# Performance work log

Measured on AMD Instinct MI355X. Metric: run time of the kernel, lower is better.

Reference implementation:

```python
import jax, jax.numpy as jnp
import numpy as np

N = 262144          # total instances (patches)
E = 512             # encoding_size
H = 256             # attention_hidden_size
NUM_BAGS = 512      # number of bags (slides); max(batch_indices)+1


def setup_inputs() -> dict:
    key = jax.random.key(0)
    k1, k2, k3, k4, k5 = jax.random.split(key, 5)
    bag_encoding = jax.random.normal(k1, (N, E), dtype=jnp.float32)
    idx = jnp.sort(jax.random.randint(k2, (N,), 0, NUM_BAGS))
    # ensure num_bags = max+1 == NUM_BAGS deterministically
    batch_indices = idx.at[0].set(0).at[-1].set(NUM_BAGS - 1)
    # kaiming-uniform-ish fan_in init scales
    Vw = jax.random.uniform(k3, (H, E), jnp.float32, -1.0, 1.0) * np.sqrt(6.0 / E)
    Vb = jnp.zeros((H,), jnp.float32)
    ww = jax.random.uniform(k4, (1, H), jnp.float32, -1.0, 1.0) * np.sqrt(6.0 / H)
    wb = jnp.zeros((1,), jnp.float32)
    dw = jax.random.uniform(k5, (2, E), jnp.float32, -1.0, 1.0) * np.sqrt(6.0 / E)
    db = jnp.zeros((2,), jnp.float32)
    return {"bag_encoding": bag_encoding, "Vw": Vw, "Vb": Vb, "ww": ww,
            "wb": wb, "dw": dw, "db": db, "batch_indices": batch_indices}


def reference(bag_encoding, Vw, Vb, ww, wb, dw, db, batch_indices):
    # attention scores: tanh(V x) -> w -> exp   [N, 1]
    v = jnp.tanh(jnp.einsum('ne,he->nh', bag_encoding, Vw) + Vb)
    alphas = jnp.exp(jnp.einsum('nh,oh->no', v, ww) + wb)  # [N, 1]
    # segment softmax denominator per bag
    sum_alphas = jax.ops.segment_sum(alphas, batch_indices, num_segments=NUM_BAGS)  # [B, 1]
    alphas = alphas / sum_alphas[batch_indices]
    # attention-weighted bag pooling
    bag_sum = jax.ops.segment_sum(alphas * bag_encoding, batch_indices, num_segments=NUM_BAGS)  # [B, E]
    logits = jnp.einsum('be,ce->bc', bag_sum, dw) + db  # [B, 2]
    return jax.nn.softmax(logits, axis=1)
```

## Files before the change

### kernel.cpp

```cpp
#include <hip/hip_runtime.h>
#include <hip/hip_bf16.h>

#define N_INST 262144
#define E_DIM  512
#define H_DIM  256
#define NBAGS  512
#define MI     32
#define XS_STRIDE 520
#define NBLOCKS 256
#define TILES_PER_BLK (N_INST / MI / NBLOCKS)

typedef __bf16 bf16x8 __attribute__((ext_vector_type(8)));
typedef float  f32x4  __attribute__((ext_vector_type(4)));

__device__ __forceinline__ float fast_tanh(float x) {
    float e = __expf(2.0f * x);
    return 1.0f - 2.0f * __builtin_amdgcn_rcpf(e + 1.0f);
}

__global__ void vw_to_bf16(const float* __restrict__ src,
                           __hip_bfloat16* __restrict__ dst) {
    int i = (blockIdx.x * 256 + threadIdx.x) * 4;
    float4 f = *(const float4*)(src + i);
    dst[i + 0] = __float2bfloat16(f.x);
    dst[i + 1] = __float2bfloat16(f.y);
    dst[i + 2] = __float2bfloat16(f.z);
    dst[i + 3] = __float2bfloat16(f.w);
}

__global__ __launch_bounds__(512, 2) void attn_persist(
    const float* __restrict__ X,
    const __hip_bfloat16* __restrict__ Vw,
    const float* __restrict__ Vb,
    const float* __restrict__ ww,
    const float* __restrict__ wb,
    const int* __restrict__ bidx,
    float* __restrict__ bag_acc,
    float* __restrict__ sum_alphas)
{
    __shared__ __hip_bfloat16 xs[2][MI][XS_STRIDE];
    __shared__ float s_part[8][MI];
    __shared__ float a_sh[MI];
    __shared__ int   bag_sh[2][MI];

    const int tid  = threadIdx.x;
    const int wave = tid >> 6;
    const int lane = tid & 63;
    const int l16  = lane & 15;
    const int kgrp = lane >> 4;

    const int tile0 = blockIdx.x * TILES_PER_BLK;

    bf16x8 breg[16][2];
    float ww_r[2], vb_r[2];
    {
        const __bf16* Vwp = (const __bf16*)Vw;
        #pragma unroll
        for (int nt = 0; nt < 2; nt++) {
            const int h = wave * 32 + nt * 16 + l16;
            ww_r[nt] = ww[h];
            vb_r[nt] = Vb[h];
            #pragma unroll
            for (int k = 0; k < 16; k++)
                breg[k][nt] = *(const bf16x8*)(Vwp + (size_t)h * E_DIM + k * 32 + kgrp * 8);
        }
    }

    const int c4 = tid & 127;
    const int r0 = tid >> 7;

    {
        const size_t i0 = (size_t)tile0 * MI;
        #pragma unroll
        for (int rr = 0; rr < 8; rr++) {
            const int r = rr * 4 + r0;
            float4 f = *(const float4*)(X + (i0 + r) * E_DIM + c4 * 4);
            __hip_bfloat16* dst = &xs[0][r][c4 * 4];
            dst[0] = __float2bfloat16(f.x);
            dst[1] = __float2bfloat16(f.y);
            dst[2] = __float2bfloat16(f.z);
            dst[3] = __float2bfloat16(f.w);
        }
        if (tid < MI) bag_sh[0][tid] = bidx[i0 + tid];
    }
    __syncthreads();

    int   cur_bag = -1;
    float col_acc = 0.f;
    float asum    = 0.f;

    int p = 0;
    for (int it = 0; it < TILES_PER_BLK; it++) {
        const size_t inst0 = (size_t)(tile0 + it) * MI;
        const bool has_next = (it + 1 < TILES_PER_BLK);

        float4 ld[8];
        if (has_next) {
            const size_t i1 = inst0 + MI;
            #pragma unroll
            for (int rr = 0; rr < 8; rr++)
                ld[rr] = *(const float4*)(X + (i1 + rr * 4 + r0) * E_DIM + c4 * 4);
        }

        f32x4 acc[2][2];
        #pragma unroll
        for (int mt = 0; mt < 2; mt++)
            #pragma unroll
            for (int nt = 0; nt < 2; nt++)
                acc[mt][nt] = (f32x4){0.f, 0.f, 0.f, 0.f};

        #pragma unroll
        for (int k = 0; k < 16; k++) {
            bf16x8 a_frag[2];
            #pragma unroll
            for (int mt = 0; mt < 2; mt++)
                a_frag[mt] = *(const bf16x8*)&xs[p][mt * 16 + l16][k * 32 + kgrp * 8];
            #pragma unroll
            for (int mt = 0; mt < 2; mt++)
                #pragma unroll
                for (int nt = 0; nt < 2; nt++)
                    acc[mt][nt] = __builtin_amdgcn_mfma_f32_16x16x32_bf16(
                        a_frag[mt], breg[k][nt], acc[mt][nt], 0, 0, 0);
        }

        if (has_next) {
            #pragma unroll
            for (int rr = 0; rr < 8; rr++) {
                const int r = rr * 4 + r0;
                __hip_bfloat16* dst = &xs[p ^ 1][r][c4 * 4];
                dst[0] = __float2bfloat16(ld[rr].x);
                dst[1] = __float2bfloat16(ld[rr].y);
                dst[2] = __float2bfloat16(ld[rr].z);
                dst[3] = __float2bfloat16(ld[rr].w);
            }
            if (tid < MI) bag_sh[p ^ 1][tid] = bidx[inst0 + MI + tid];
        }

        #pragma unroll
        for (int mt = 0; mt < 2; mt++) {
            #pragma unroll
            for (int r = 0; r < 4; r++) {
                float t = 0.f;
                #pragma unroll
                for (int nt = 0; nt < 2; nt++)
                    t += ww_r[nt] * fast_tanh(acc[mt][nt][r] + vb_r[nt]);
                #pragma unroll
                for (int off = 1; off < 16; off <<= 1)
                    t += __shfl_xor(t, off, 64);
                if (l16 == 0)
                    s_part[wave][mt * 16 + kgrp * 4 + r] = t;
            }
        }
        __syncthreads();

        if (tid < MI) {
            float s = wb[0];
            #pragma unroll
            for (int w = 0; w < 8; w++) s += s_part[w][tid];
            a_sh[tid] = __expf(s);
        }
        __syncthreads();

        for (int i = 0; i < MI; i++) {
            const int b = bag_sh[p][i];
            if (b != cur_bag) {
                if (cur_bag >= 0) {
                    atomicAdd(&bag_acc[(size_t)cur_bag * E_DIM + tid], col_acc);
                    if (tid == 0) atomicAdd(&sum_alphas[cur_bag], asum);
                }
                cur_bag = b; col_acc = 0.f; asum = 0.f;
            }
            const float a = a_sh[i];
            col_acc += a * __bfloat162float(xs[p][i][tid]);
            asum    += a;
        }
        __syncthreads();
        p ^= 1;
    }

    if (cur_bag >= 0) {
        atomicAdd(&bag_acc[(size_t)cur_bag * E_DIM + tid], col_acc);
        if (tid == 0) atomicAdd(&sum_alphas[cur_bag], asum);
    }
}

__global__ void finalize(const float* __restrict__ bag_acc,
                         const float* __restrict__ sum_alphas,
                         const float* __restrict__ dw,
                         const float* __restrict__ db,
                         float* __restrict__ out) {
    const int b = blockIdx.x;
    const int lane = threadIdx.x;
    const float sa = sum_alphas[b];
    const float inv = (sa > 0.f) ? (1.f / sa) : 0.f;
    float l0 = 0.f, l1 = 0.f;
    for (int e = lane; e < E_DIM; e += 64) {
        const float bs = bag_acc[(size_t)b * E_DIM + e] * inv;
        l0 += bs * dw[e];
        l1 += bs * dw[E_DIM + e];
    }
    for (int off = 32; off; off >>= 1) {
        l0 += __shfl_xor(l0, off, 64);
        l1 += __shfl_xor(l1, off, 64);
    }
    if (lane == 0) {
        l0 += db[0];
        l1 += db[1];
        const float m  = fmaxf(l0, l1);
        const float e0 = expf(l0 - m), e1 = expf(l1 - m);
        const float is = 1.f / (e0 + e1);
        out[b * 2 + 0] = e0 * is;
        out[b * 2 + 1] = e1 * is;
    }
}

extern "C" void kernel_launch(void* const* d_in, const int* in_sizes, int n_in,
                              void* d_out, int out_size, void* d_ws, size_t ws_size,
                              hipStream_t stream) {
    const float* X   = (const float*)d_in[0];
    const float* Vwf = (const float*)d_in[1];
    const float* Vb  = (const float*)d_in[2];
    const float* ww  = (const float*)d_in[3];
    const float* wb  = (const float*)d_in[4];
    const float* dw  = (const float*)d_in[5];
    const float* db  = (const float*)d_in[6];
    const int*  bidx = (const int*)d_in[7];
    float* out = (float*)d_out;

    __hip_bfloat16* Vwb = (__hip_bfloat16*)d_ws;
    float* bag_acc    = (float*)((char*)d_ws + (size_t)H_DIM * E_DIM * 2);
    float* sum_alphas = bag_acc + (size_t)NBAGS * E_DIM;

    hipMemsetAsync(bag_acc, 0, ((size_t)NBAGS * E_DIM + NBAGS) * sizeof(float), stream);
    vw_to_bf16<<<H_DIM * E_DIM / 1024, 256, 0, stream>>>(Vwf, Vwb);
    attn_persist<<<NBLOCKS, 512, 0, stream>>>(X, Vwb, Vb, ww, wb, bidx,
                                              bag_acc, sum_alphas);
    finalize<<<NBAGS, 64, 0, stream>>>(bag_acc, sum_alphas, dw, db, out);
}
```

Measured before the change: 759.8 us.

## Stage X tiles into LDS with async global_load_lds and XOR swizzle

Replaces register-staged global loads followed by bf16 conversion stores with direct global-to-LDS asynchronous 16-byte loads that keep X in fp32, using an XOR swizzle on column chunks to avoid bank conflicts. The bf16 conversion moves into the MFMA fragment load, and the pooling reads exact fp32 values from the swizzled layout. This removes register pressure and VALU store work in the prefetch path and lets loads overlap compute without occupying VGPRs. In exchange LDS use doubles to 128KB per block, which may limit occupancy under launch_bounds(512,2), and each MFMA fragment now needs two LDS reads plus conversions.

```diff
diff --git a/kernel.cpp b/kernel.cpp
--- a/kernel.cpp
+++ b/kernel.cpp
@@ -6,7 +6,6 @@
 #define H_DIM  256
 #define NBAGS  512
 #define MI     32
-#define XS_STRIDE 520
 #define NBLOCKS 256
 #define TILES_PER_BLK (N_INST / MI / NBLOCKS)
 
@@ -16,6 +15,13 @@
 __device__ __forceinline__ float fast_tanh(float x) {
     float e = __expf(2.0f * x);
     return 1.0f - 2.0f * __builtin_amdgcn_rcpf(e + 1.0f);
+}
+
+__device__ __forceinline__ void async_stage16(const float* g, float* l) {
+    __builtin_amdgcn_global_load_lds(
+        (const __attribute__((address_space(1))) void*)(const void*)g,
+        (__attribute__((address_space(3))) void*)(void*)l,
+        16, 0, 0);
 }
 
 __global__ void vw_to_bf16(const float* __restrict__ src,
@@ -38,7 +44,7 @@
     float* __restrict__ bag_acc,
     float* __restrict__ sum_alphas)
 {
-    __shared__ __hip_bfloat16 xs[2][MI][XS_STRIDE];
+    __shared__ float xsb[2][MI * E_DIM];
     __shared__ float s_part[8][MI];
     __shared__ float a_sh[MI];
     __shared__ int   bag_sh[2][MI];
@@ -48,6 +54,7 @@
     const int lane = tid & 63;
     const int l16  = lane & 15;
     const int kgrp = lane >> 4;
+    const int sw   = l16 & 7;
 
     const int tile0 = blockIdx.x * TILES_PER_BLK;
 
@@ -66,40 +73,46 @@
         }
     }
 
-    const int c4 = tid & 127;
-    const int r0 = tid >> 7;
-
     {
         const size_t i0 = (size_t)tile0 * MI;
         #pragma unroll
-        for (int rr = 0; rr < 8; rr++) {
-            const int r = rr * 4 + r0;
-            float4 f = *(const float4*)(X + (i0 + r) * E_DIM + c4 * 4);
-            __hip_bfloat16* dst = &xs[0][r][c4 * 4];
-            dst[0] = __float2bfloat16(f.x);
-            dst[1] = __float2bfloat16(f.y);
-            dst[2] = __float2bfloat16(f.z);
-            dst[3] = __float2bfloat16(f.w);
+        for (int j = 0; j < 8; j++) {
+            const int idx  = wave * 8 + j;
+            const int r    = idx >> 1;
+            const int half = idx & 1;
+            const int c    = half * 64 + (lane ^ (r & 7));
+            async_stage16(X + (i0 + r) * E_DIM + c * 4,
+                          &xsb[0][r * E_DIM + half * 256]);
         }
         if (tid < MI) bag_sh[0][tid] = bidx[i0 + tid];
     }
+    asm volatile("s_waitcnt vmcnt(0)" ::: "memory");
+    __builtin_amdgcn_sched_barrier(0);
     __syncthreads();
 
     int   cur_bag = -1;
     float col_acc = 0.f;
     float asum    = 0.f;
+    const int colchunk = tid >> 2;
+    const int colrem   = tid & 3;
 
     int p = 0;
     for (int it = 0; it < TILES_PER_BLK; it++) {
         const size_t inst0 = (size_t)(tile0 + it) * MI;
         const bool has_next = (it + 1 < TILES_PER_BLK);
 
-        float4 ld[8];
         if (has_next) {
             const size_t i1 = inst0 + MI;
             #pragma unroll
-            for (int rr = 0; rr < 8; rr++)
-                ld[rr] = *(const float4*)(X + (i1 + rr * 4 + r0) * E_DIM + c4 * 4);
+            for (int j = 0; j < 8; j++) {
+                const int idx  = wave * 8 + j;
+                const int r    = idx >> 1;
+                const int half = idx & 1;
+                const int c    = half * 64 + (lane ^ (r & 7));
+                async_stage16(X + (i1 + r) * E_DIM + c * 4,
+                              &xsb[p ^ 1][r * E_DIM + half * 256]);
+            }
+            if (tid < MI) bag_sh[p ^ 1][tid] = bidx[i1 + tid];
         }
 
         f32x4 acc[2][2];
@@ -109,31 +122,31 @@
             for (int nt = 0; nt < 2; nt++)
                 acc[mt][nt] = (f32x4){0.f, 0.f, 0.f, 0.f};
 
+        const float* xp = &xsb[p][0];
         #pragma unroll
         for (int k = 0; k < 16; k++) {
-            bf16x8 a_frag[2];
-            #pragma unroll
-            for (int mt = 0; mt < 2; mt++)
-                a_frag[mt] = *(const bf16x8*)&xs[p][mt * 16 + l16][k * 32 + kgrp * 8];
+            const int c0 = k * 8 + kgrp * 2;
+            const int o0 = ((c0     ^ sw) << 2);
+            const int o1 = (((c0+1) ^ sw) << 2);
+            bf16x8 afr[2];
+            #pragma unroll
+            for (int mt = 0; mt < 2; mt++) {
+                const float* rowp = xp + (mt * 16 + l16) * E_DIM;
+                f32x4 lo = *(const f32x4*)(rowp + o0);
+                f32x4 hi = *(const f32x4*)(rowp + o1);
+                bf16x8 fr;
+                fr[0] = (__bf16)lo[0]; fr[1] = (__bf16)lo[1];
+                fr[2] = (__bf16)lo[2]; fr[3] = (__bf16)lo[3];
+                fr[4] = (__bf16)hi[0]; fr[5] = (__bf16)hi[1];
+                fr[6] = (__bf16)hi[2]; fr[7] = (__bf16)hi[3];
+                afr[mt] = fr;
+            }
             #pragma unroll
             for (int mt = 0; mt < 2; mt++)
                 #pragma unroll
                 for (int nt = 0; nt < 2; nt++)
                     acc[mt][nt] = __builtin_amdgcn_mfma_f32_16x16x32_bf16(
-                        a_frag[mt], breg[k][nt], acc[mt][nt], 0, 0, 0);
-        }
-
-        if (has_next) {
-            #pragma unroll
-            for (int rr = 0; rr < 8; rr++) {
-                const int r = rr * 4 + r0;
-                __hip_bfloat16* dst = &xs[p ^ 1][r][c4 * 4];
-                dst[0] = __float2bfloat16(ld[rr].x);
-                dst[1] = __float2bfloat16(ld[rr].y);
-                dst[2] = __float2bfloat16(ld[rr].z);
-                dst[3] = __float2bfloat16(ld[rr].w);
-            }
-            if (tid < MI) bag_sh[p ^ 1][tid] = bidx[inst0 + MI + tid];
+                        afr[mt], breg[k][nt], acc[mt][nt], 0, 0, 0);
         }
 
         #pragma unroll
@@ -171,9 +184,13 @@
                 cur_bag = b; col_acc = 0.f; asum = 0.f;
             }
             const float a = a_sh[i];
-            col_acc += a * __bfloat162float(xs[p][i][tid]);
+            const float x = xp[i * E_DIM + ((colchunk ^ (i & 7)) << 2) + colrem];
+            col_acc += a * x;
             asum    += a;
         }
+
+        asm volatile("s_waitcnt vmcnt(0)" ::: "memory");
+        __builtin_amdgcn_sched_barrier(0);
         __syncthreads();
         p ^= 1;
     }
```

New measurement: 799.0 us. +5.2%, slower.
